# Optimization experiments

Measured on AMD Instinct MI355X. Metric: run time of the kernel, lower is better.

## Reference

```python
import jax, jax.numpy as jnp
import numpy as np

NUM_WIRES = 14
N_LAYERS = 2
BATCH = 256
DIM = 2 ** NUM_WIRES


def setup_inputs() -> dict:
    key = jax.random.key(0)
    k1, k2, k3 = jax.random.split(key, 3)
    s = jax.random.normal(k1, (BATCH, DIM), dtype=jnp.float32)
    # StatePrep requires normalized amplitudes
    s = s / jnp.linalg.norm(s, axis=1, keepdims=True)
    params = jax.random.normal(k2, (N_LAYERS, NUM_WIRES, 3), dtype=jnp.float32)
    head_w = jax.random.normal(k3, (1, NUM_WIRES), dtype=jnp.float32) / np.sqrt(NUM_WIRES)
    head_b = jnp.zeros((1,), dtype=jnp.float32)
    return {"state_batch": s, "params": params, "head_w": head_w, "head_b": head_b}


def _ry(t):
    c = jnp.cos(t / 2).astype(jnp.complex64)
    s = jnp.sin(t / 2).astype(jnp.complex64)
    return jnp.stack([jnp.stack([c, -s]), jnp.stack([s, c])])


def _rz(t):
    tc = t.astype(jnp.complex64)
    e_m = jnp.exp(-0.5j * tc)
    e_p = jnp.exp(0.5j * tc)
    z = jnp.zeros((), jnp.complex64)
    return jnp.stack([jnp.stack([e_m, z]), jnp.stack([z, e_p])])


def _rx(t):
    c = jnp.cos(t / 2).astype(jnp.complex64)
    s = (-1j) * jnp.sin(t / 2).astype(jnp.complex64)
    return jnp.stack([jnp.stack([c, s]), jnp.stack([s, c])])


def _apply_1q(psi, U, wire):
    # psi: (B, 2, 2, ..., 2); contract 2x2 gate on axis wire+1 across the batch
    out = jnp.tensordot(U, psi, axes=([1], [wire + 1]))
    return jnp.moveaxis(out, 0, wire + 1)


def _apply_cnot(psi, control, target):
    # flip target axis where control bit == 1
    shape = [1] * psi.ndim
    shape[control + 1] = 2
    mask = (jnp.arange(2) == 1).reshape(shape)
    return jnp.where(mask, jnp.flip(psi, axis=target + 1), psi)


def _circuit(state_c, params):
    psi = state_c.reshape((BATCH,) + (2,) * NUM_WIRES)
    for layer in range(N_LAYERS):
        for w in range(NUM_WIRES):
            psi = _apply_1q(psi, _ry(params[layer, w, 0]), w)
            psi = _apply_1q(psi, _rz(params[layer, w, 1]), w)
            psi = _apply_cnot(psi, w, (w + 1) % NUM_WIRES)
            psi = _apply_1q(psi, _rx(params[layer, w, 2]), w)
    probs = (psi.real ** 2 + psi.imag ** 2).reshape(BATCH, DIM)
    # <Z_w> = sum over basis states of prob * (+1/-1 depending on bit of wire w)
    basis = jnp.arange(DIM)
    shifts = NUM_WIRES - 1 - jnp.arange(NUM_WIRES)  # wire 0 is the MSB axis
    signs = 1.0 - 2.0 * ((basis[None, :] >> shifts[:, None]) & 1).astype(jnp.float32)
    return probs @ signs.T  # (B, NUM_WIRES)


def reference(state_batch, params, head_w, head_b):
    feats = _circuit(state_batch.astype(jnp.complex64), params)  # (B, NUM_WIRES)
    return feats @ head_w[0] + head_b[0]  # (B,)
```

## Files before the change

kernel.cpp:

```cpp
#include <hip/hip_runtime.h>
#include <math.h>

typedef float v2f __attribute__((ext_vector_type(2)));

constexpr int NW = 14;
constexpr int DIM = 1 << NW;
constexpr int BATCH = 256;
constexpr int NT = 1024;

__device__ __host__ constexpr int swz2(int i) {
    return i ^ ((i >> 4) & 15) ^ ((i >> 8) & 15) ^ ((i >> 12) & 3);
}

template<int Q0,int Q1,int Q2,int Q3,int Q4,int Q5,int Q6,int Q7,int Q8,int Q9>
__device__ __forceinline__ int scat10(int t) {
    return ((t & 1) << Q0) | (((t >> 1) & 1) << Q1) | (((t >> 2) & 1) << Q2) |
           (((t >> 3) & 1) << Q3) | (((t >> 4) & 1) << Q4) | (((t >> 5) & 1) << Q5) |
           (((t >> 6) & 1) << Q6) | (((t >> 7) & 1) << Q7) | (((t >> 8) & 1) << Q8) |
           (((t >> 9) & 1) << Q9);
}

template<int JW, int JT>
__device__ __forceinline__ void gate_u(v2f (&pr)[8], v2f (&pi)[8],
                                       float cy, float sy, float c1, float s1,
                                       float cx, float sx)
{
    constexpr int BW = 1 << JW, BT = 1 << JT, JF = 3 - JW - JT;
    #pragma unroll
    for (int m = 0; m < 2; ++m) {
        const int l00 = m << JF;
        const int iA = l00, iB = l00 | BW, iC = l00 | BT, iD = l00 | BW | BT;

        v2f a00r = pr[iA], a00i = pi[iA];
        v2f a10r = pr[iB], a10i = pi[iB];
        v2f a01r = pr[iC], a01i = pi[iC];
        v2f a11r = pr[iD], a11i = pi[iD];

        v2f v0r = cy*a00r - sy*a10r, v0i = cy*a00i - sy*a10i;
        v2f v1r = sy*a00r + cy*a10r, v1i = sy*a00i + cy*a10i;
        v2f u0r = cy*a01r - sy*a11r, u0i = cy*a01i - sy*a11i;
        v2f u1r = sy*a01r + cy*a11r, u1i = sy*a01i + cy*a11i;

        v2f b00r = c1*v0r + s1*v0i, b00i = c1*v0i - s1*v0r;
        v2f b10r = c1*v1r - s1*v1i, b10i = c1*v1i + s1*v1r;
        v2f b01r = c1*u0r + s1*u0i, b01i = c1*u0i - s1*u0r;
        v2f b11r = c1*u1r - s1*u1i, b11i = c1*u1i + s1*u1r;

        v2f o00r = cx*b00r + sx*b11i, o00i = cx*b00i - sx*b11r;
        v2f o10r = sx*b00i + cx*b11r, o10i = cx*b11i - sx*b00r;
        v2f o01r = cx*b01r + sx*b10i, o01i = cx*b01i - sx*b10r;
        v2f o11r = sx*b01i + cx*b10r, o11i = cx*b10i - sx*b01r;

        pr[iA] = o00r; pi[iA] = o00i;
        pr[iB] = o10r; pi[iB] = o10i;
        pr[iC] = o01r; pi[iC] = o01i;
        pr[iD] = o11r; pi[iD] = o11i;
    }
}

template<int JT>
__device__ __forceinline__ void gate_w(v2f (&pr)[8], v2f (&pi)[8],
                                       float cy, float sy, float c1, float s1,
                                       float cx, float sx)
{
    constexpr int BT = 1 << JT;
    constexpr int jA = (JT == 0) ? 1 : 0, jB = (JT == 2) ? 1 : 2;
    const v2f K1 = {cy, sy};
    const v2f K2 = {-sy, cy};
    const v2f Zs = {s1, -s1};
    #pragma unroll
    for (int m = 0; m < 4; ++m) {
        const int l00 = ((m & 1) << jA) | (((m >> 1) & 1) << jB);
        const int iA = l00, iB = l00 | BT;
        v2f Ar = pr[iA], Ai = pi[iA];
        v2f Br = pr[iB], Bi = pi[iB];

        v2f vAr = K1*Ar.xx + K2*Ar.yy;
        v2f vAi = K1*Ai.xx + K2*Ai.yy;
        v2f vBr = K1*Br.xx + K2*Br.yy;
        v2f vBi = K1*Bi.xx + K2*Bi.yy;

        v2f bAr = c1*vAr + Zs*vAi;
        v2f bAi = c1*vAi - Zs*vAr;
        v2f bBr = c1*vBr + Zs*vBi;
        v2f bBi = c1*vBi - Zs*vBr;

        v2f t1  = {bAr.x, bBr.y};
        v2f t1p = {bBr.x, bAr.y};
        v2f t2  = {bAi.x, bBi.y};
        v2f t2p = {bBi.x, bAi.y};
        pr[iA] = cx*t1  + sx*t2.yx;
        pi[iA] = cx*t2  - sx*t1.yx;
        pr[iB] = cx*t1p + sx*t2p.yx;
        pi[iB] = cx*t2p - sx*t1p.yx;
    }
}

template<int J>
__device__ __forceinline__ void swap_l5(v2f (&pr)[8], v2f (&pi)[8]) {
    constexpr int jA = (J == 0) ? 1 : 0, jB = (J == 2) ? 1 : 2;
    #pragma unroll
    for (int m = 0; m < 4; ++m) {
        const int l0 = ((m & 1) << jA) | (((m >> 1) & 1) << jB);
        const int l1 = l0 | (1 << J);
        { float a=pr[l0].x, c=pr[l1].x; asm("s_nop 1\n\tv_permlane32_swap_b32 %0, %1":"+v"(a),"+v"(c)); pr[l0].x=a; pr[l1].x=c; }
        { float a=pr[l0].y, c=pr[l1].y; asm("s_nop 1\n\tv_permlane32_swap_b32 %0, %1":"+v"(a),"+v"(c)); pr[l0].y=a; pr[l1].y=c; }
        { float a=pi[l0].x, c=pi[l1].x; asm("s_nop 1\n\tv_permlane32_swap_b32 %0, %1":"+v"(a),"+v"(c)); pi[l0].x=a; pi[l1].x=c; }
        { float a=pi[l0].y, c=pi[l1].y; asm("s_nop 1\n\tv_permlane32_swap_b32 %0, %1":"+v"(a),"+v"(c)); pi[l0].y=a; pi[l1].y=c; }
    }
}

template<int J>
__device__ __forceinline__ void swap_l4(v2f (&pr)[8], v2f (&pi)[8]) {
    constexpr int jA = (J == 0) ? 1 : 0, jB = (J == 2) ? 1 : 2;
    #pragma unroll
    for (int m = 0; m < 4; ++m) {
        const int l0 = ((m & 1) << jA) | (((m >> 1) & 1) << jB);
        const int l1 = l0 | (1 << J);
        { float a=pr[l0].x, c=pr[l1].x; asm("s_nop 1\n\tv_permlane16_swap_b32 %0, %1":"+v"(a),"+v"(c)); pr[l0].x=a; pr[l1].x=c; }
        { float a=pr[l0].y, c=pr[l1].y; asm("s_nop 1\n\tv_permlane16_swap_b32 %0, %1":"+v"(a),"+v"(c)); pr[l0].y=a; pr[l1].y=c; }
        { float a=pi[l0].x, c=pi[l1].x; asm("s_nop 1\n\tv_permlane16_swap_b32 %0, %1":"+v"(a),"+v"(c)); pi[l0].x=a; pi[l1].x=c; }
        { float a=pi[l0].y, c=pi[l1].y; asm("s_nop 1\n\tv_permlane16_swap_b32 %0, %1":"+v"(a),"+v"(c)); pi[l0].y=a; pi[l1].y=c; }
    }
}

template<int S0,int S1,int S2,int PP>
__device__ __forceinline__ void lds_store(float2* cs,
                                          const v2f (&pr)[8], const v2f (&pi)[8], int sb) {
    #pragma unroll
    for (int k = 0; k < 8; ++k) {
        const int off = ((k & 1) << S0) | (((k >> 1) & 1) << S1) | (((k >> 2) & 1) << S2);
        cs[sb ^ swz2(off)]             = float2{pr[k].x, pi[k].x};
        cs[sb ^ swz2(off | (1 << PP))] = float2{pr[k].y, pi[k].y};
    }
}

template<int S0,int S1,int S2,int PP>
__device__ __forceinline__ void lds_load(const float2* cs,
                                         v2f (&pr)[8], v2f (&pi)[8], int sb) {
    #pragma unroll
    for (int k = 0; k < 8; ++k) {
        const int off = ((k & 1) << S0) | (((k >> 1) & 1) << S1) | (((k >> 2) & 1) << S2);
        const float2 a0 = cs[sb ^ swz2(off)];
        const float2 a1 = cs[sb ^ swz2(off | (1 << PP))];
        pr[k] = v2f{a0.x, a1.x};
        pi[k] = v2f{a0.y, a1.y};
    }
}

__global__ __launch_bounds__(NT, 1) void qsim(const float* __restrict__ state,
                                              const float* __restrict__ params,
                                              const float* __restrict__ head_w,
                                              const float* __restrict__ head_b,
                                              float* __restrict__ out)
{
    __shared__ float2 cs[DIM];
    __shared__ float2 csv[NW * 3 * 2];
    __shared__ float partial[NT / 64];

    const int t = threadIdx.x;
    const int b = blockIdx.x;

    v2f pr[8], pi[8];

    const float* __restrict__ sp = state + (size_t)b * DIM;
    const int tbA = scat10<0,1,2,3,8,9,4,5,6,7>(t);
    #pragma unroll
    for (int k = 0; k < 8; ++k) {
        const int base = tbA | (k << 10);
        pr[k] = v2f{sp[base], sp[base | (1 << 13)]};
        pi[k] = v2f{0.0f, 0.0f};
    }

    if (t < NW * 3 * 2) {
        float sv, cv;
        sincosf(params[t] * 0.5f, &sv, &cv);
        csv[t] = make_float2(cv, sv);
    }
    __syncthreads();

#define GU(JW, JT, G) do {                                              \
        float2 vy = csv[(G)*3+0], vz = csv[(G)*3+1], vx = csv[(G)*3+2]; \
        gate_u<JW, JT>(pr, pi, vy.x, vy.y, vz.x, vz.y, vx.x, vx.y);     \
    } while (0)
#define GW(JT, G) do {                                                  \
        float2 vy = csv[(G)*3+0], vz = csv[(G)*3+1], vx = csv[(G)*3+2]; \
        gate_w<JT>(pr, pi, vy.x, vy.y, vz.x, vz.y, vx.x, vx.y);         \
    } while (0)

    GW(2, 0);
    GU(2, 1, 1);
    GU(1, 0, 2);
    swap_l5<2>(pr, pi);
    GU(0, 2, 3);
    swap_l4<1>(pr, pi);
    GU(2, 1, 4);
    lds_store<10,8,9,13>(cs, pr, pi, swz2(scat10<0,1,2,3,11,12,4,5,6,7>(t)));
    __syncthreads();

    const int sbB = swz2(scat10<0,1,2,9,3,4,10,11,12,13>(t));
    lds_load<5,6,7,8>(cs, pr, pi, sbB);
    GW(2, 5);
    GU(2, 1, 6);
    GU(1, 0, 7);
    swap_l5<2>(pr, pi);
    GU(0, 2, 8);
    swap_l4<1>(pr, pi);
    GU(2, 1, 9);
    lds_store<5,3,4,8>(cs, pr, pi, swz2(scat10<0,1,2,9,6,7,10,11,12,13>(t)));
    __syncthreads();

    const int sbC = swz2(scat10<4,5,6,7,9,13,8,10,11,12>(t));
    lds_load<0,1,2,3>(cs, pr, pi, sbC);
    GW(2, 10);
    GU(2, 1, 11);
    GU(1, 0, 12);
    swap_l5<2>(pr, pi);
    GU(0, 2, 13);
    lds_store<0,1,13,3>(cs, pr, pi, swz2(scat10<4,5,6,7,9,2,8,10,11,12>(t)));
    __syncthreads();

    lds_load<10,11,12,13>(cs, pr, pi, swz2(tbA));
    GW(2, 14);
    GU(2, 1, 15);
    GU(1, 0, 16);
    swap_l5<2>(pr, pi);
    GU(0, 2, 17);
    swap_l4<1>(pr, pi);
    GU(2, 1, 18);
    lds_store<10,8,9,13>(cs, pr, pi, swz2(scat10<0,1,2,3,11,12,4,5,6,7>(t)));
    __syncthreads();

    lds_load<5,6,7,8>(cs, pr, pi, sbB);
    GW(2, 19);
    GU(2, 1, 20);
    GU(1, 0, 21);
    swap_l5<2>(pr, pi);
    GU(0, 2, 22);
    swap_l4<1>(pr, pi);
    GU(2, 1, 23);
    lds_store<5,3,4,8>(cs, pr, pi, swz2(scat10<0,1,2,9,6,7,10,11,12,13>(t)));
    __syncthreads();

    lds_load<0,1,2,3>(cs, pr, pi, sbC);
    GW(2, 24);
    GU(2, 1, 25);
    GU(1, 0, 26);
    swap_l5<2>(pr, pi);
    GU(0, 2, 27);

    float hw[NW];
    #pragma unroll
    for (int w = 0; w < NW; ++w) hw[w] = head_w[w];

    float gbase = 0.0f;
    gbase += (t & 1)   ? -hw[9]  : hw[9];
    gbase += (t & 2)   ? -hw[8]  : hw[8];
    gbase += (t & 4)   ? -hw[7]  : hw[7];
    gbase += (t & 8)   ? -hw[6]  : hw[6];
    gbase += (t & 16)  ? -hw[4]  : hw[4];
    gbase += (t & 32)  ? -hw[11] : hw[11];
    gbase += (t & 64)  ? -hw[5]  : hw[5];
    gbase += (t & 128) ? -hw[3]  : hw[3];
    gbase += (t & 256) ? -hw[2]  : hw[2];
    gbase += (t & 512) ? -hw[1]  : hw[1];

    v2f acc2 = {0.0f, 0.0f};
    #pragma unroll
    for (int k = 0; k < 8; ++k) {
        float g = gbase;
        g += (k & 1) ? -hw[13] : hw[13];
        g += (k & 2) ? -hw[12] : hw[12];
        g += (k & 4) ? -hw[0]  : hw[0];
        v2f gv = {g + hw[10], g - hw[10]};
        acc2 += (pr[k]*pr[k] + pi[k]*pi[k]) * gv;
    }
    float acc = acc2.x + acc2.y;

    #pragma unroll
    for (int off = 32; off > 0; off >>= 1) acc += __shfl_down(acc, off);
    if ((t & 63) == 0) partial[t >> 6] = acc;
    __syncthreads();
    if (t == 0) {
        float tot = 0.0f;
        #pragma unroll
        for (int k = 0; k < NT / 64; ++k) tot += partial[k];
        out[b] = tot + head_b[0];
    }
#undef GU
#undef GW
}

extern "C" void kernel_launch(void* const* d_in, const int* in_sizes, int n_in,
                              void* d_out, int out_size, void* d_ws, size_t ws_size,
                              hipStream_t stream) {
    const float* state  = (const float*)d_in[0];
    const float* params = (const float*)d_in[1];
    const float* head_w = (const float*)d_in[2];
    const float* head_b = (const float*)d_in[3];
    float* outp = (float*)d_out;
    qsim<<<BATCH, NT, 0, stream>>>(state, params, head_w, head_b, outp);
}
```

Measured before the change: 36.74 us.

## Split LDS state into planar re/im arrays with paired-lane layout and new swizzle

Replaces the interleaved complex float2 shared buffer with separate real and imaginary arrays. The state is now laid out so that each thread's v2f lane pair holds adjacent amplitudes, which allows 64-bit vector LDS accesses and float2 global loads. The gate and stage schedule is reorganised around this: the gate_w variant is removed and stages become uniform, with six LDS exchanges whose wire mappings and final sign mapping are rewritten to match. Gate coefficients are forced into scalar registers with readfirstlane. The extra exchange stage and the new swizzle could bring more barriers or bank conflicts.

```diff
diff --git a/kernel.cpp b/kernel.cpp
--- a/kernel.cpp
+++ b/kernel.cpp
@@ -8,8 +8,12 @@
 constexpr int BATCH = 256;
 constexpr int NT = 1024;
 
-__device__ __host__ constexpr int swz2(int i) {
-    return i ^ ((i >> 4) & 15) ^ ((i >> 8) & 15) ^ ((i >> 12) & 3);
+__device__ __host__ constexpr int swz(int i) {
+    return i ^ (((i >> 5) & 15) << 1) ^ (((i >> 9) & 15) << 1) ^ (((i >> 13) & 1) << 1);
+}
+
+__device__ __forceinline__ float rfl(float x) {
+    return __int_as_float(__builtin_amdgcn_readfirstlane(__float_as_int(x)));
 }
 
 template<int Q0,int Q1,int Q2,int Q3,int Q4,int Q5,int Q6,int Q7,int Q8,int Q9>
@@ -55,44 +59,6 @@
         pr[iB] = o10r; pi[iB] = o10i;
         pr[iC] = o01r; pi[iC] = o01i;
         pr[iD] = o11r; pi[iD] = o11i;
-    }
-}
-
-template<int JT>
-__device__ __forceinline__ void gate_w(v2f (&pr)[8], v2f (&pi)[8],
-                                       float cy, float sy, float c1, float s1,
-                                       float cx, float sx)
-{
-    constexpr int BT = 1 << JT;
-    constexpr int jA = (JT == 0) ? 1 : 0, jB = (JT == 2) ? 1 : 2;
-    const v2f K1 = {cy, sy};
-    const v2f K2 = {-sy, cy};
-    const v2f Zs = {s1, -s1};
-    #pragma unroll
-    for (int m = 0; m < 4; ++m) {
-        const int l00 = ((m & 1) << jA) | (((m >> 1) & 1) << jB);
-        const int iA = l00, iB = l00 | BT;
-        v2f Ar = pr[iA], Ai = pi[iA];
-        v2f Br = pr[iB], Bi = pi[iB];
-
-        v2f vAr = K1*Ar.xx + K2*Ar.yy;
-        v2f vAi = K1*Ai.xx + K2*Ai.yy;
-        v2f vBr = K1*Br.xx + K2*Br.yy;
-        v2f vBi = K1*Bi.xx + K2*Bi.yy;
-
-        v2f bAr = c1*vAr + Zs*vAi;
-        v2f bAi = c1*vAi - Zs*vAr;
-        v2f bBr = c1*vBr + Zs*vBi;
-        v2f bBi = c1*vBi - Zs*vBr;
-
-        v2f t1  = {bAr.x, bBr.y};
-        v2f t1p = {bBr.x, bAr.y};
-        v2f t2  = {bAi.x, bBi.y};
-        v2f t2p = {bBi.x, bAi.y};
-        pr[iA] = cx*t1  + sx*t2.yx;
-        pi[iA] = cx*t2  - sx*t1.yx;
-        pr[iB] = cx*t1p + sx*t2p.yx;
-        pi[iB] = cx*t2p - sx*t1p.yx;
     }
 }
 
@@ -124,27 +90,53 @@
     }
 }
 
-template<int S0,int S1,int S2,int PP>
-__device__ __forceinline__ void lds_store(float2* cs,
-                                          const v2f (&pr)[8], const v2f (&pi)[8], int sb) {
-    #pragma unroll
-    for (int k = 0; k < 8; ++k) {
-        const int off = ((k & 1) << S0) | (((k >> 1) & 1) << S1) | (((k >> 2) & 1) << S2);
-        cs[sb ^ swz2(off)]             = float2{pr[k].x, pi[k].x};
-        cs[sb ^ swz2(off | (1 << PP))] = float2{pr[k].y, pi[k].y};
-    }
-}
-
-template<int S0,int S1,int S2,int PP>
-__device__ __forceinline__ void lds_load(const float2* cs,
-                                         v2f (&pr)[8], v2f (&pi)[8], int sb) {
-    #pragma unroll
-    for (int k = 0; k < 8; ++k) {
-        const int off = ((k & 1) << S0) | (((k >> 1) & 1) << S1) | (((k >> 2) & 1) << S2);
-        const float2 a0 = cs[sb ^ swz2(off)];
-        const float2 a1 = cs[sb ^ swz2(off | (1 << PP))];
-        pr[k] = v2f{a0.x, a1.x};
-        pi[k] = v2f{a0.y, a1.y};
+template<int S0,int S1,int S2>
+__device__ __forceinline__ void store64(float* re, float* im,
+                                        const v2f (&pr)[8], const v2f (&pi)[8], int sb) {
+    #pragma unroll
+    for (int k = 0; k < 8; ++k) {
+        const int c = swz(((k & 1) << S0) | (((k >> 1) & 1) << S1) | (((k >> 2) & 1) << S2));
+        const int a = sb ^ c;
+        *(v2f*)(re + a) = pr[k];
+        *(v2f*)(im + a) = pi[k];
+    }
+}
+
+template<int S0,int S1,int S2>
+__device__ __forceinline__ void load64(const float* re, const float* im,
+                                       v2f (&pr)[8], v2f (&pi)[8], int sb) {
+    #pragma unroll
+    for (int k = 0; k < 8; ++k) {
+        const int c = swz(((k & 1) << S0) | (((k >> 1) & 1) << S1) | (((k >> 2) & 1) << S2));
+        const int a = sb ^ c;
+        pr[k] = *(const v2f*)(re + a);
+        pi[k] = *(const v2f*)(im + a);
+    }
+}
+
+template<int S0,int S1,int S2>
+__device__ __forceinline__ void store32(float* re, float* im,
+                                        const v2f (&pr)[8], const v2f (&pi)[8], int sb) {
+    #pragma unroll
+    for (int k = 0; k < 8; ++k) {
+        const int cc = ((k & 1) << S0) | (((k >> 1) & 1) << S1) | (((k >> 2) & 1) << S2);
+        const int a0 = sb ^ swz(cc);
+        const int a1 = sb ^ swz(cc | 32);
+        re[a0] = pr[k].x; re[a1] = pr[k].y;
+        im[a0] = pi[k].x; im[a1] = pi[k].y;
+    }
+}
+
+template<int S0,int S1,int S2>
+__device__ __forceinline__ void load32(const float* re, const float* im,
+                                       v2f (&pr)[8], v2f (&pi)[8], int sb) {
+    #pragma unroll
+    for (int k = 0; k < 8; ++k) {
+        const int cc = ((k & 1) << S0) | (((k >> 1) & 1) << S1) | (((k >> 2) & 1) << S2);
+        const int a0 = sb ^ swz(cc);
+        const int a1 = sb ^ swz(cc | 32);
+        pr[k].x = re[a0]; pr[k].y = re[a1];
+        pi[k].x = im[a0]; pi[k].y = im[a1];
     }
 }
 
@@ -154,7 +146,8 @@
                                               const float* __restrict__ head_b,
                                               float* __restrict__ out)
 {
-    __shared__ float2 cs[DIM];
+    __shared__ float re[DIM];
+    __shared__ float im[DIM];
     __shared__ float2 csv[NW * 3 * 2];
     __shared__ float partial[NT / 64];
 
@@ -163,12 +156,13 @@
 
     v2f pr[8], pi[8];
 
-    const float* __restrict__ sp = state + (size_t)b * DIM;
-    const int tbA = scat10<0,1,2,3,8,9,4,5,6,7>(t);
-    #pragma unroll
-    for (int k = 0; k < 8; ++k) {
-        const int base = tbA | (k << 10);
-        pr[k] = v2f{sp[base], sp[base | (1 << 13)]};
+    const float2* __restrict__ sp2 = (const float2*)(state + (size_t)b * DIM);
+    const int tb1 = scat10<1,2,3,4,9,10,5,6,7,8>(t);
+    #pragma unroll
+    for (int k = 0; k < 8; ++k) {
+        const int idx = tb1 | ((k & 1) << 11) | (((k >> 1) & 1) << 12) | (((k >> 2) & 1) << 13);
+        const float2 v = sp2[idx >> 1];
+        pr[k] = v2f{v.x, v.y};
         pi[k] = v2f{0.0f, 0.0f};
     }
 
@@ -181,98 +175,101 @@
 
 #define GU(JW, JT, G) do {                                              \
         float2 vy = csv[(G)*3+0], vz = csv[(G)*3+1], vx = csv[(G)*3+2]; \
-        gate_u<JW, JT>(pr, pi, vy.x, vy.y, vz.x, vz.y, vx.x, vx.y);     \
+        gate_u<JW, JT>(pr, pi, rfl(vy.x), rfl(vy.y), rfl(vz.x),         \
+                       rfl(vz.y), rfl(vx.x), rfl(vx.y));                \
     } while (0)
-#define GW(JT, G) do {                                                  \
-        float2 vy = csv[(G)*3+0], vz = csv[(G)*3+1], vx = csv[(G)*3+2]; \
-        gate_w<JT>(pr, pi, vy.x, vy.y, vz.x, vz.y, vx.x, vx.y);         \
-    } while (0)
-
-    GW(2, 0);
-    GU(2, 1, 1);
-    GU(1, 0, 2);
-    swap_l5<2>(pr, pi);
-    GU(0, 2, 3);
-    swap_l4<1>(pr, pi);
+
+    GU(2, 1, 0);
+    GU(1, 0, 1);
+    swap_l5<2>(pr, pi);
+    GU(0, 2, 2);
+    swap_l4<1>(pr, pi);
+    GU(2, 1, 3);
+    store64<11,9,10>(re, im, pr, pi, swz(scat10<1,2,3,4,12,13,5,6,7,8>(t)));
+    __syncthreads();
+
+    load64<7,8,9>(re, im, pr, pi, swz(scat10<1,2,3,4,5,6,13,12,11,10>(t)));
     GU(2, 1, 4);
-    lds_store<10,8,9,13>(cs, pr, pi, swz2(scat10<0,1,2,3,11,12,4,5,6,7>(t)));
-    __syncthreads();
-
-    const int sbB = swz2(scat10<0,1,2,9,3,4,10,11,12,13>(t));
-    lds_load<5,6,7,8>(cs, pr, pi, sbB);
-    GW(2, 5);
-    GU(2, 1, 6);
-    GU(1, 0, 7);
-    swap_l5<2>(pr, pi);
-    GU(0, 2, 8);
-    swap_l4<1>(pr, pi);
-    GU(2, 1, 9);
-    lds_store<5,3,4,8>(cs, pr, pi, swz2(scat10<0,1,2,9,6,7,10,11,12,13>(t)));
-    __syncthreads();
-
-    const int sbC = swz2(scat10<4,5,6,7,9,13,8,10,11,12>(t));
-    lds_load<0,1,2,3>(cs, pr, pi, sbC);
-    GW(2, 10);
+    GU(1, 0, 5);
+    swap_l5<2>(pr, pi);
+    GU(0, 2, 6);
+    swap_l4<1>(pr, pi);
+    GU(2, 1, 7);
+    store64<7,5,6>(re, im, pr, pi, swz(scat10<1,2,3,4,8,9,13,12,11,10>(t)));
+    __syncthreads();
+
+    load64<3,4,5>(re, im, pr, pi, swz(scat10<13,6,7,8,1,2,12,11,10,9>(t)));
+    GU(2, 1, 8);
+    GU(1, 0, 9);
+    swap_l5<2>(pr, pi);
+    GU(0, 2, 10);
+    swap_l4<1>(pr, pi);
     GU(2, 1, 11);
-    GU(1, 0, 12);
-    swap_l5<2>(pr, pi);
-    GU(0, 2, 13);
-    lds_store<0,1,13,3>(cs, pr, pi, swz2(scat10<4,5,6,7,9,2,8,10,11,12>(t)));
-    __syncthreads();
-
-    lds_load<10,11,12,13>(cs, pr, pi, swz2(tbA));
-    GW(2, 14);
+    store64<3,1,2>(re, im, pr, pi, swz(scat10<13,6,7,8,4,5,12,11,10,9>(t)));
+    __syncthreads();
+
+    load32<13,0,1>(re, im, pr, pi, swz(scat10<2,3,4,9,11,12,10,8,7,6>(t)));
+    GU(2, 1, 12);
+    GU(1, 0, 13);
+    swap_l5<2>(pr, pi);
+    GU(0, 2, 14);
+    swap_l4<1>(pr, pi);
     GU(2, 1, 15);
-    GU(1, 0, 16);
-    swap_l5<2>(pr, pi);
-    GU(0, 2, 17);
-    swap_l4<1>(pr, pi);
-    GU(2, 1, 18);
-    lds_store<10,8,9,13>(cs, pr, pi, swz2(scat10<0,1,2,3,11,12,4,5,6,7>(t)));
-    __syncthreads();
-
-    lds_load<5,6,7,8>(cs, pr, pi, sbB);
-    GW(2, 19);
+    store32<13,11,12>(re, im, pr, pi, swz(scat10<2,3,4,9,0,1,10,8,7,6>(t)));
+    __syncthreads();
+
+    load64<9,10,11>(re, im, pr, pi, swz(scat10<1,2,3,4,7,8,13,12,6,5>(t)));
+    GU(2, 1, 16);
+    GU(1, 0, 17);
+    swap_l5<2>(pr, pi);
+    GU(0, 2, 18);
+    swap_l4<1>(pr, pi);
+    GU(2, 1, 19);
+    store64<9,7,8>(re, im, pr, pi, swz(scat10<1,2,3,4,10,11,13,12,6,5>(t)));
+    __syncthreads();
+
+    load64<5,6,7>(re, im, pr, pi, swz(scat10<1,2,11,8,3,4,13,12,10,9>(t)));
     GU(2, 1, 20);
     GU(1, 0, 21);
     swap_l5<2>(pr, pi);
     GU(0, 2, 22);
     swap_l4<1>(pr, pi);
     GU(2, 1, 23);
-    lds_store<5,3,4,8>(cs, pr, pi, swz2(scat10<0,1,2,9,6,7,10,11,12,13>(t)));
-    __syncthreads();
-
-    lds_load<0,1,2,3>(cs, pr, pi, sbC);
-    GW(2, 24);
-    GU(2, 1, 25);
-    GU(1, 0, 26);
-    swap_l5<2>(pr, pi);
-    GU(0, 2, 27);
+    store64<5,3,4>(re, im, pr, pi, swz(scat10<1,2,11,8,6,7,13,12,10,9>(t)));
+    __syncthreads();
+
+    load32<1,2,3>(re, im, pr, pi, swz(scat10<9,10,11,12,13,0,8,7,6,4>(t)));
+    GU(2, 1, 24);
+    GU(1, 0, 25);
+    swap_l5<2>(pr, pi);
+    GU(0, 2, 26);
+    swap_l4<1>(pr, pi);
+    GU(2, 1, 27);
 
     float hw[NW];
     #pragma unroll
     for (int w = 0; w < NW; ++w) hw[w] = head_w[w];
 
     float gbase = 0.0f;
-    gbase += (t & 1)   ? -hw[9]  : hw[9];
-    gbase += (t & 2)   ? -hw[8]  : hw[8];
-    gbase += (t & 4)   ? -hw[7]  : hw[7];
-    gbase += (t & 8)   ? -hw[6]  : hw[6];
-    gbase += (t & 16)  ? -hw[4]  : hw[4];
-    gbase += (t & 32)  ? -hw[11] : hw[11];
+    gbase += (t & 1)   ? -hw[4]  : hw[4];
+    gbase += (t & 2)   ? -hw[3]  : hw[3];
+    gbase += (t & 4)   ? -hw[2]  : hw[2];
+    gbase += (t & 8)   ? -hw[1]  : hw[1];
+    gbase += (t & 16)  ? -hw[11] : hw[11];
+    gbase += (t & 32)  ? -hw[10] : hw[10];
     gbase += (t & 64)  ? -hw[5]  : hw[5];
-    gbase += (t & 128) ? -hw[3]  : hw[3];
-    gbase += (t & 256) ? -hw[2]  : hw[2];
-    gbase += (t & 512) ? -hw[1]  : hw[1];
+    gbase += (t & 128) ? -hw[6]  : hw[6];
+    gbase += (t & 256) ? -hw[7]  : hw[7];
+    gbase += (t & 512) ? -hw[9]  : hw[9];
 
     v2f acc2 = {0.0f, 0.0f};
     #pragma unroll
     for (int k = 0; k < 8; ++k) {
         float g = gbase;
-        g += (k & 1) ? -hw[13] : hw[13];
-        g += (k & 2) ? -hw[12] : hw[12];
-        g += (k & 4) ? -hw[0]  : hw[0];
-        v2f gv = {g + hw[10], g - hw[10]};
+        g += (k & 1) ? -hw[12] : hw[12];
+        g += (k & 2) ? -hw[0]  : hw[0];
+        g += (k & 4) ? -hw[13] : hw[13];
+        v2f gv = {g + hw[8], g - hw[8]};
         acc2 += (pr[k]*pr[k] + pi[k]*pi[k]) * gv;
     }
     float acc = acc2.x + acc2.y;
@@ -288,7 +285,6 @@
         out[b] = tot + head_b[0];
     }
 #undef GU
-#undef GW
 }
 
 extern "C" void kernel_launch(void* const* d_in, const int* in_sizes, int n_in,
```

Measured after the change: 37.45 us. Within noise of the previous version (+1.9%).
